# Optimization experiments

Hardware: AMD Instinct MI355X
Metric: run time of the kernel (lower is better)

## Reference

```python
import jax, jax.numpy as jnp
import numpy as np

B, P, D, F = 2048, 16, 1024, 512  # batch, n_prompt, dim, fusion_dim
S = 2 * P  # sequence length
H = D // 2  # classifier hidden
LN_EPS = 1e-5


def _ln_relu(y, g, b):
    mu = jnp.mean(y, axis=-1, keepdims=True)
    var = jnp.mean(jnp.square(y - mu), axis=-1, keepdims=True)
    return jax.nn.relu((y - mu) * jax.lax.rsqrt(var + LN_EPS) * g + b)


def setup_inputs() -> dict:
    key = jax.random.key(0)
    ks = jax.random.split(key, 24)
    n = lambda k, shp, scale: jax.random.normal(k, shp, dtype=jnp.float32) * scale
    return {
        "q": n(ks[0], (B, S, D), 1.0),
        # nn.MultiheadAttention (1 head, batch_first)
        "in_proj_w": n(ks[1], (3 * D, D), 1.0 / np.sqrt(D)),
        "in_proj_b": jnp.zeros((3 * D,), jnp.float32),
        "out_w": n(ks[2], (D, D), 1.0 / np.sqrt(D)),
        "out_b": jnp.zeros((D,), jnp.float32),
        # 32 per-position classifiers, stacked: Linear(D,H)+ReLU+Linear(H,1)+ReLU
        "cls_w1": n(ks[3], (S, H, D), 1.0 / np.sqrt(D)),
        "cls_b1": jnp.zeros((S, H), jnp.float32),
        "cls_w2": n(ks[4], (S, H), 1.0 / np.sqrt(H)),
        "cls_b2": jnp.zeros((S,), jnp.float32),
        # fusion / projector heads: Linear(D,F)+LayerNorm(F)+ReLU
        "fus_w": n(ks[5], (F, D), 1.0 / np.sqrt(D)),
        "fus_b": jnp.zeros((F,), jnp.float32),
        "fus_g": jnp.ones((F,), jnp.float32),
        "fus_be": jnp.zeros((F,), jnp.float32),
        "pa_w": n(ks[6], (F, D), 1.0 / np.sqrt(D)),
        "pa_b": jnp.zeros((F,), jnp.float32),
        "pa_g": jnp.ones((F,), jnp.float32),
        "pa_be": jnp.zeros((F,), jnp.float32),
        "pv_w": n(ks[7], (F, D), 1.0 / np.sqrt(D)),
        "pv_b": jnp.zeros((F,), jnp.float32),
        "pv_g": jnp.ones((F,), jnp.float32),
        "pv_be": jnp.zeros((F,), jnp.float32),
    }


def reference(q, in_proj_w, in_proj_b, out_w, out_b,
              cls_w1, cls_b1, cls_w2, cls_b2,
              fus_w, fus_b, fus_g, fus_be,
              pa_w, pa_b, pa_g, pa_be,
              pv_w, pv_b, pv_g, pv_be):
    # --- single-head self-attention (nn.MultiheadAttention, eval mode) ---
    wq, wk, wv = jnp.split(in_proj_w, 3, axis=0)
    bq, bk, bv = jnp.split(in_proj_b, 3, axis=0)
    qp = jnp.einsum('bsd,ed->bse', q, wq) + bq
    kp = jnp.einsum('bsd,ed->bse', q, wk) + bk
    vp = jnp.einsum('bsd,ed->bse', q, wv) + bv
    scores = jnp.einsum('bse,bte->bst', qp, kp) / jnp.sqrt(jnp.float32(D))
    attn = jax.nn.softmax(scores, axis=-1)
    q_att = jnp.einsum('bst,bte->bse', attn, vp)
    q_att = jnp.einsum('bse,de->bsd', q_att, out_w) + out_b

    # --- per-position tiny classifiers, batched over the 32 slots ---
    h = jax.nn.relu(jnp.einsum('bsd,shd->bsh', q, cls_w1) + cls_b1)  # [B,S,H]
    d = jax.nn.relu(jnp.einsum('bsh,sh->bs', h, cls_w2) + cls_b2)    # [B,S]

    d_a = jax.nn.softmax(d[:, :P], axis=-1)
    d_v = jax.nn.softmax(d[:, P:], axis=-1)
    audio = jnp.einsum('bsd,bs->bd', q_att[:, :P, :], d_a)
    video = jnp.einsum('bsd,bs->bd', q_att[:, P:, :], d_v)
    fusion = (audio + video) * 0.5

    fusion_h = _ln_relu(fusion @ fus_w.T + fus_b, fus_g, fus_be)
    fusion_a = _ln_relu(audio @ pa_w.T + pa_b, pa_g, pa_be)
    fusion_v = _ln_relu(video @ pv_w.T + pv_b, pv_g, pv_be)
    return (fusion_h, fusion_a, fusion_v, d_a, d_v)
```

## Files before the change

kernel.cpp:

```cpp
#include <hip/hip_runtime.h>

#define Bdim 2048
#define Sdim 32
#define Ddim 1024
#define Fdim 512
#define Hdim 512

typedef __bf16 bf16_t;
typedef __bf16 bf16x8 __attribute__((ext_vector_type(8)));
typedef __bf16 bf16x4 __attribute__((ext_vector_type(4)));
typedef float  f32x4  __attribute__((ext_vector_type(4)));

#define BM 128
#define BN 128
#define BK 32

__device__ __forceinline__ void gll16(const bf16_t* g, bf16_t* l) {
  __builtin_amdgcn_global_load_lds((const __attribute__((address_space(1))) void*)g,
                                   (__attribute__((address_space(3))) void*)l,
                                   16, 0, 0);
}

__device__ __forceinline__ int swz32(int row, int k) {
  return row * 32 + (((((k >> 3) ^ ((row >> 1) & 3))) << 3) | (k & 7));
}

__global__ void k_cvt_all(const float* __restrict__ q, const float* __restrict__ ipw,
                          const float* __restrict__ ow, const float* __restrict__ cw1,
                          const float* __restrict__ fusw, const float* __restrict__ paw,
                          const float* __restrict__ pvw,
                          bf16_t* __restrict__ q16, bf16_t* __restrict__ w16,
                          bf16_t* __restrict__ ow16, bf16_t* __restrict__ cls16,
                          bf16_t* __restrict__ hw16) {
  long v = (long)blockIdx.x * 256 + threadIdx.x;
  const float* s; bf16_t* d; long off;
  if (v < 16777216L)      { s = q;    d = q16;            off = 0; }
  else if (v < 17563648L) { s = ipw;  d = w16;            off = 16777216L; }
  else if (v < 17825792L) { s = ow;   d = ow16;           off = 17563648L; }
  else if (v < 22020096L) { s = cw1;  d = cls16;          off = 17825792L; }
  else if (v < 22151168L) { s = fusw; d = hw16;           off = 22020096L; }
  else if (v < 22282240L) { s = paw;  d = hw16 + 524288;  off = 22151168L; }
  else                    { s = pvw;  d = hw16 + 1048576; off = 22282240L; }
  long i = (v - off) * 4;
  float4 t = *(const float4*)(s + i);
  bf16x4 o;
  o[0] = (bf16_t)t.x; o[1] = (bf16_t)t.y; o[2] = (bf16_t)t.z; o[3] = (bf16_t)t.w;
  *(bf16x4*)(d + i) = o;
}

__global__ void k_bias_pre(const float* __restrict__ ipw, const float* __restrict__ ipb,
                           const float* __restrict__ ow, const float* __restrict__ ob,
                           float* __restrict__ u, float* __restrict__ w,
                           float* __restrict__ bp, float* __restrict__ c0) {
  int blk = blockIdx.x, tid = threadIdx.x;
  if (blk < 4) {
    int d = blk * 256 + tid;
    float acc = 0.f;
    #pragma unroll 8
    for (int e = 0; e < Ddim; ++e) acc += ipw[(long)e * Ddim + d] * ipb[Ddim + e];
    u[d] = acc;
  } else if (blk < 8) {
    int d = (blk - 4) * 256 + tid;
    float acc = 0.f;
    #pragma unroll 8
    for (int e = 0; e < Ddim; ++e) acc += ipw[(long)(Ddim + e) * Ddim + d] * ipb[e];
    w[d] = acc;
  } else if (blk < 136) {
    int o = (blk - 8) * 8 + (tid >> 5);
    int l = tid & 31;
    float acc = 0.f;
    #pragma unroll 4
    for (int e = l; e < Ddim; e += 32) acc += ow[(long)o * Ddim + e] * ipb[2 * Ddim + e];
    #pragma unroll
    for (int m = 1; m < 32; m <<= 1) acc += __shfl_xor(acc, m);
    if (l == 0) bp[o] = acc + ob[o];
  } else {
    __shared__ float red[256];
    float acc = 0.f;
    for (int e = tid; e < Ddim; e += 256) acc += ipb[e] * ipb[Ddim + e];
    red[tid] = acc;
    __syncthreads();
    for (int off = 128; off; off >>= 1) {
      if (tid < off) red[tid] += red[tid + off];
      __syncthreads();
    }
    if (tid == 0) c0[0] = red[0];
  }
}

template<int AT, int BT>
__device__ __forceinline__ void gemm_tile(const bf16_t* __restrict__ A, long lda,
                                          const bf16_t* __restrict__ Bt, long ldb,
                                          long m0, long n0, int K,
                                          bf16_t* sa, bf16_t* sb, f32x4 acc[4][4]) {
  const int tid  = threadIdx.x;
  const int wave = tid >> 6;
  const int lane = tid & 63;
  const int quad = lane >> 4;
  const int l16  = lane & 15;
  const int wm = (wave & 1) * 64;
  const int wn = (wave >> 1) * 64;

  for (int kt = 0; kt < K; kt += BK) {
    __syncthreads();
    if constexpr (AT == 0) {
      #pragma unroll
      for (int r = 0; r < 2; ++r) {
        int L = r * 256 + tid;
        int row = L >> 2, cs = L & 3;
        int csrc = cs ^ ((row >> 1) & 3);
        gll16(A + (m0 + row) * lda + kt + csrc * 8, sa + (long)(r * 256 + wave * 64) * 8);
      }
    } else {
      #pragma unroll
      for (int r = 0; r < 2; ++r) {
        int L = r * 256 + tid;
        int gk = L >> 4, gm = (L & 15) * 8;
        bf16x8 v = *(const bf16x8*)(A + (long)(kt + gk) * lda + m0 + gm);
        #pragma unroll
        for (int j = 0; j < 8; ++j) sa[swz32(gm + j, gk)] = v[j];
      }
    }
    if constexpr (BT == 0) {
      #pragma unroll
      for (int r = 0; r < 2; ++r) {
        int L = r * 256 + tid;
        int row = L >> 2, cs = L & 3;
        int csrc = cs ^ ((row >> 1) & 3);
        gll16(Bt + (n0 + row) * ldb + kt + csrc * 8, sb + (long)(r * 256 + wave * 64) * 8);
      }
    } else {
      #pragma unroll
      for (int r = 0; r < 2; ++r) {
        int L = r * 256 + tid;
        int gk = L >> 4, gn = (L & 15) * 8;
        bf16x8 v = *(const bf16x8*)(Bt + (long)(kt + gk) * ldb + n0 + gn);
        #pragma unroll
        for (int j = 0; j < 8; ++j) sb[swz32(gn + j, gk)] = v[j];
      }
    }
    __syncthreads();
    bf16x8 af[4], bfr[4];
    #pragma unroll
    for (int i = 0; i < 4; ++i) {
      int row = wm + i * 16 + l16;
      af[i] = *(const bf16x8*)(sa + row * 32 + ((quad ^ ((row >> 1) & 3)) << 3));
    }
    #pragma unroll
    for (int j = 0; j < 4; ++j) {
      int row = wn + j * 16 + l16;
      bfr[j] = *(const bf16x8*)(sb + row * 32 + ((quad ^ ((row >> 1) & 3)) << 3));
    }
    #pragma unroll
    for (int i = 0; i < 4; ++i)
      #pragma unroll
      for (int j = 0; j < 4; ++j)
        acc[i][j] = __builtin_amdgcn_mfma_f32_16x16x32_bf16(bfr[j], af[i], acc[i][j], 0, 0, 0);
  }
}

template<int AT, int BT>
__global__ __launch_bounds__(256) void k_gemm_bf16(
    const bf16_t* __restrict__ A, long lda, long sAz,
    const bf16_t* __restrict__ Bt, long ldb, long sBz,
    bf16_t* __restrict__ C, long ldc, long sCz,
    const float* __restrict__ bias, int K) {
  __shared__ bf16_t sa[BM * BK];
  __shared__ bf16_t sb[BN * BK];
  long n0 = (long)blockIdx.x * BN;
  long m0 = (long)blockIdx.y * BM;
  long z  = blockIdx.z;
  const bf16_t* Az = A + z * sAz;
  const bf16_t* Bz = Bt + z * sBz;
  bf16_t* Cz = C + z * sCz;
  f32x4 acc[4][4];
  #pragma unroll
  for (int i = 0; i < 4; ++i)
    #pragma unroll
    for (int j = 0; j < 4; ++j) acc[i][j] = (f32x4){0.f, 0.f, 0.f, 0.f};
  gemm_tile<AT, BT>(Az, lda, Bz, ldb, m0, n0, K, sa, sb, acc);
  const int tid = threadIdx.x, wave = tid >> 6, lane = tid & 63;
  const int quad = lane >> 4, l16 = lane & 15;
  const int wm = (wave & 1) * 64, wn = (wave >> 1) * 64;
  #pragma unroll
  for (int i = 0; i < 4; ++i) {
    long row = m0 + wm + i * 16 + l16;
    #pragma unroll
    for (int j = 0; j < 4; ++j) {
      long col = n0 + wn + j * 16 + quad * 4;
      f32x4 b4 = bias ? *(const f32x4*)(bias + col) : (f32x4){0.f, 0.f, 0.f, 0.f};
      bf16x4 o;
      #pragma unroll
      for (int r = 0; r < 4; ++r) o[r] = (bf16_t)(acc[i][j][r] + b4[r]);
      *(bf16x4*)(Cz + row * ldc + col) = o;
    }
  }
}

__global__ __launch_bounds__(256) void k_gemm_f32(
    const bf16_t* __restrict__ A, long lda, long sAz,
    const bf16_t* __restrict__ Bt, long ldb, long sBz,
    float* __restrict__ C, long ldc, long sCz, int K) {
  __shared__ bf16_t sa[BM * BK];
  __shared__ bf16_t sb[BN * BK];
  long n0 = (long)blockIdx.x * BN;
  long m0 = (long)blockIdx.y * BM;
  long z  = blockIdx.z;
  const bf16_t* Az = A + z * sAz;
  const bf16_t* Bz = Bt + z * sBz;
  float* Cz = C + z * sCz;
  f32x4 acc[4][4];
  #pragma unroll
  for (int i = 0; i < 4; ++i)
    #pragma unroll
    for (int j = 0; j < 4; ++j) acc[i][j] = (f32x4){0.f, 0.f, 0.f, 0.f};
  gemm_tile<0, 0>(Az, lda, Bz, ldb, m0, n0, K, sa, sb, acc);
  const int tid = threadIdx.x, wave = tid >> 6, lane = tid & 63;
  const int quad = lane >> 4, l16 = lane & 15;
  const int wm = (wave & 1) * 64, wn = (wave >> 1) * 64;
  #pragma unroll
  for (int i = 0; i < 4; ++i) {
    long row = m0 + wm + i * 16 + l16;
    #pragma unroll
    for (int j = 0; j < 4; ++j) {
      long col = n0 + wn + j * 16 + quad * 4;
      *(f32x4*)(Cz + row * ldc + col) = acc[i][j];
    }
  }
}

__global__ __launch_bounds__(256, 2) void k_gemm_big(
    const bf16_t* __restrict__ A, const bf16_t* __restrict__ Bt,
    bf16_t* __restrict__ C) {
  __shared__ bf16_t sa[128 * 64];
  __shared__ bf16_t sb[256 * 64];
  const int tid = threadIdx.x, wave = tid >> 6, lane = tid & 63;
  const int quad = lane >> 4, l16 = lane & 15;
  int lin = blockIdx.y * 4 + blockIdx.x;
  int c = lin & 7, j0 = lin >> 3;
  long m0 = ((long)c * 64 + (j0 >> 2)) * 128;
  long n0 = (long)(j0 & 3) * 256;
  const int wm = (wave & 1) * 64;
  const int wn = (wave >> 1) * 128;
  f32x4 acc[4][8];
  #pragma unroll
  for (int i = 0; i < 4; ++i)
    #pragma unroll
    for (int j = 0; j < 8; ++j) acc[i][j] = (f32x4){0.f, 0.f, 0.f, 0.f};
  for (int kt = 0; kt < 1024; kt += 64) {
    __syncthreads();
    #pragma unroll
    for (int r = 0; r < 4; ++r) {
      int L = r * 256 + tid;
      int row = L >> 3, cs = L & 7;
      int csrc = cs ^ ((row >> 1) & 7);
      gll16(A + (m0 + row) * 1024 + kt + csrc * 8, sa + (long)(r * 256 + wave * 64) * 8);
    }
    #pragma unroll
    for (int r = 0; r < 8; ++r) {
      int L = r * 256 + tid;
      int row = L >> 3, cs = L & 7;
      int csrc = cs ^ ((row >> 1) & 7);
      gll16(Bt + (n0 + row) * 1024 + kt + csrc * 8, sb + (long)(r * 256 + wave * 64) * 8);
    }
    __syncthreads();
    #pragma unroll
    for (int h = 0; h < 2; ++h) {
      bf16x8 af[4], bfr[8];
      #pragma unroll
      for (int i = 0; i < 4; ++i) {
        int row = wm + i * 16 + l16;
        int cc = h * 4 + quad;
        af[i] = *(const bf16x8*)(sa + row * 64 + ((cc ^ ((row >> 1) & 7)) << 3));
      }
      #pragma unroll
      for (int j = 0; j < 8; ++j) {
        int row = wn + j * 16 + l16;
        int cc = h * 4 + quad;
        bfr[j] = *(const bf16x8*)(sb + row * 64 + ((cc ^ ((row >> 1) & 7)) << 3));
      }
      #pragma unroll
      for (int i = 0; i < 4; ++i)
        #pragma unroll
        for (int j = 0; j < 8; ++j)
          acc[i][j] = __builtin_amdgcn_mfma_f32_16x16x32_bf16(bfr[j], af[i], acc[i][j], 0, 0, 0);
    }
  }
  #pragma unroll
  for (int i = 0; i < 4; ++i) {
    long row = m0 + wm + i * 16 + l16;
    #pragma unroll
    for (int j = 0; j < 8; ++j) {
      long col = n0 + wn + j * 16 + quad * 4;
      bf16x4 o;
      #pragma unroll
      for (int r = 0; r < 4; ++r) o[r] = (bf16_t)(acc[i][j][r]);
      *(bf16x4*)(C + row * 1024 + col) = o;
    }
  }
}

__global__ __launch_bounds__(256) void k_gemm_cls(
    const bf16_t* __restrict__ q16, const bf16_t* __restrict__ w1,
    const float* __restrict__ b1, const float* __restrict__ w2,
    float* __restrict__ dsum) {
  __shared__ bf16_t sa[BM * BK];
  __shared__ bf16_t sb[BN * BK];
  int lin = ((int)blockIdx.z * 16 + blockIdx.y) * 4 + blockIdx.x;
  int c = lin & 7, j0 = lin >> 3;
  int p = c + 8 * (j0 >> 2);
  long n0 = (long)(j0 & 3) * BN;
  int s = p >> 4;
  long m0 = (long)(p & 15) * BM;
  const bf16_t* A  = q16 + (long)s * Ddim;
  const bf16_t* Bt = w1 + (long)s * Hdim * Ddim;
  f32x4 acc[4][4];
  #pragma unroll
  for (int i = 0; i < 4; ++i)
    #pragma unroll
    for (int j = 0; j < 4; ++j) acc[i][j] = (f32x4){0.f, 0.f, 0.f, 0.f};
  gemm_tile<0, 0>(A, (long)Sdim * Ddim, Bt, Ddim, m0, n0, Ddim, sa, sb, acc);
  const int tid = threadIdx.x, wave = tid >> 6, lane = tid & 63;
  const int quad = lane >> 4, l16 = lane & 15;
  const int wm = (wave & 1) * 64, wn = (wave >> 1) * 64;
  const float* b1s = b1 + (long)s * Hdim;
  const float* w2s = w2 + (long)s * Hdim;
  #pragma unroll
  for (int i = 0; i < 4; ++i) {
    float vsum = 0.f;
    #pragma unroll
    for (int j = 0; j < 4; ++j) {
      long col = n0 + wn + j * 16 + quad * 4;
      f32x4 b4 = *(const f32x4*)(b1s + col);
      f32x4 w4 = *(const f32x4*)(w2s + col);
      #pragma unroll
      for (int r = 0; r < 4; ++r)
        vsum += fmaxf(acc[i][j][r] + b4[r], 0.f) * w4[r];
    }
    vsum += __shfl_xor(vsum, 16);
    vsum += __shfl_xor(vsum, 32);
    if (lane < 16) {
      long row = m0 + wm + i * 16 + l16;
      atomicAdd(&dsum[row * Sdim + s], vsum);
    }
  }
}

__global__ void k_finalize_d(const float* __restrict__ dsum, const float* __restrict__ cb2,
                             float* __restrict__ daws, float* __restrict__ out_da,
                             float* __restrict__ out_dv) {
  int t = blockIdx.x * 256 + threadIdx.x;
  int b = t >> 5, s = t & 31;
  float v = fmaxf(dsum[t] + cb2[s], 0.f);
  float m = v;
  #pragma unroll
  for (int mask = 1; mask < 16; mask <<= 1) m = fmaxf(m, __shfl_xor(m, mask));
  float e = __expf(v - m);
  float sum = e;
  #pragma unroll
  for (int mask = 1; mask < 16; mask <<= 1) sum += __shfl_xor(sum, mask);
  float r = e / sum;
  daws[t] = r;
  if (s < 16) out_da[b * 16 + s] = r;
  else        out_dv[b * 16 + (s - 16)] = r;
}

#define QPAD 264
__global__ __launch_bounds__(256) void k_attn_pool(
    const bf16_t* __restrict__ q16, const bf16_t* __restrict__ G16,
    const float* __restrict__ daws, const float* __restrict__ u,
    const float* __restrict__ wv, const float* __restrict__ c0p,
    bf16_t* __restrict__ pooled) {
  __shared__ bf16_t qc[32 * QPAD];
  __shared__ bf16_t gc[32 * QPAD];
  __shared__ float sc[32][33];
  __shared__ float qup[32][8], qwp[32][8];
  __shared__ float quL[32], qwL[32], caL[32], cvL[32], daL[16], dvL[16];
  const int tid = threadIdx.x, wave = tid >> 6, lane = tid & 63;
  const int quad = lane >> 4, l16 = lane & 15;
  const long b = blockIdx.x;
  const bf16_t* qb = q16 + b * (Sdim * Ddim);
  const bf16_t* gb = G16 + b * (Sdim * Ddim);
  if (tid < 32) {
    float dval = daws[b * Sdim + tid];
    if (tid < 16) daL[tid] = dval; else dvL[tid - 16] = dval;
  }
  qup[tid >> 3][tid & 7] = 0.f;
  qwp[tid >> 3][tid & 7] = 0.f;
  const int ti = wave & 1, tj = wave >> 1;
  f32x4 acc = (f32x4){0.f, 0.f, 0.f, 0.f};
  for (int kc = 0; kc < Ddim; kc += 256) {
    __syncthreads();
    #pragma unroll
    for (int r = 0; r < 4; ++r) {
      int L = r * 256 + tid;
      int row = L >> 5, koff = (L & 31) * 8;
      *(bf16x8*)(qc + row * QPAD + koff) = *(const bf16x8*)(qb + (long)row * Ddim + kc + koff);
      *(bf16x8*)(gc + row * QPAD + koff) = *(const bf16x8*)(gb + (long)row * Ddim + kc + koff);
    }
    __syncthreads();
    #pragma unroll
    for (int kk = 0; kk < 8; ++kk) {
      bf16x8 a  = *(const bf16x8*)(gc + (ti * 16 + l16) * QPAD + kk * 32 + quad * 8);
      bf16x8 bb = *(const bf16x8*)(qc + (tj * 16 + l16) * QPAD + kk * 32 + quad * 8);
      acc = __builtin_amdgcn_mfma_f32_16x16x32_bf16(a, bb, acc, 0, 0, 0);
    }
    {
      int s2 = tid & 31, sl = tid >> 5;
      float pu = 0.f, pw = 0.f;
      const bf16_t* qrow = qc + s2 * QPAD + sl * 32;
      const float* ub = u + kc + sl * 32;
      const float* wb = wv + kc + sl * 32;
      #pragma unroll
      for (int kb = 0; kb < 4; ++kb) {
        bf16x8 qv = *(const bf16x8*)(qrow + kb * 8);
        f32x4 u0 = *(const f32x4*)(ub + kb * 8);
        f32x4 u1 = *(const f32x4*)(ub + kb * 8 + 4);
        f32x4 w0 = *(const f32x4*)(wb + kb * 8);
        f32x4 w1 = *(const f32x4*)(wb + kb * 8 + 4);
        #pragma unroll
        for (int e = 0; e < 4; ++e) {
          pu += (float)qv[e] * u0[e] + (float)qv[e + 4] * u1[e];
          pw += (float)qv[e] * w0[e] + (float)qv[e + 4] * w1[e];
        }
      }
      qup[s2][sl] += pu;
      qwp[s2][sl] += pw;
    }
  }
  __syncthreads();
  if (tid < 32) {
    float a0 = 0.f, a1 = 0.f;
    for (int k = 0; k < 8; ++k) { a0 += qup[tid][k]; a1 += qwp[tid][k]; }
    quL[tid] = a0; qwL[tid] = a1;
  }
  __syncthreads();
  {
    float c00 = c0p[0];
    int col = tj * 16 + l16;
    #pragma unroll
    for (int r = 0; r < 4; ++r) {
      int row = ti * 16 + quad * 4 + r;
      sc[row][col] = (acc[r] + quL[row] + qwL[col] + c00) * 0.03125f;
    }
  }
  __syncthreads();
  if (tid < 32) {
    float mx = -1e30f;
    for (int t = 0; t < 32; ++t) mx = fmaxf(mx, sc[tid][t]);
    float sum = 0.f;
    for (int t = 0; t < 32; ++t) { float e = __expf(sc[tid][t] - mx); sc[tid][t] = e; sum += e; }
    float inv = 1.f / sum;
    for (int t = 0; t < 32; ++t) sc[tid][t] *= inv;
  }
  __syncthreads();
  if (tid < 32) {
    float a0 = 0.f, a1 = 0.f;
    for (int s2 = 0; s2 < 16; ++s2) a0 += daL[s2] * sc[s2][tid];
    for (int s2 = 0; s2 < 16; ++s2) a1 += dvL[s2] * sc[16 + s2][tid];
    caL[tid] = a0; cvL[tid] = a1;
  }
  __syncthreads();
  {
    int d0 = tid * 4;
    float ap[4] = {0.f, 0.f, 0.f, 0.f}, vp[4] = {0.f, 0.f, 0.f, 0.f};
    for (int t = 0; t < 32; ++t) {
      float ca = caL[t], cv = cvL[t];
      bf16x4 qv = *(const bf16x4*)(qb + (long)t * Ddim + d0);
      #pragma unroll
      for (int e = 0; e < 4; ++e) {
        float x = (float)qv[e];
        ap[e] += ca * x;
        vp[e] += cv * x;
      }
    }
    bf16x4 pf, pa, pv;
    #pragma unroll
    for (int e = 0; e < 4; ++e) {
      pf[e] = (bf16_t)(0.5f * (ap[e] + vp[e]));
      pa[e] = (bf16_t)ap[e];
      pv[e] = (bf16_t)vp[e];
    }
    *(bf16x4*)(pooled + b * 3072 + d0)        = pf;
    *(bf16x4*)(pooled + b * 3072 + 1024 + d0) = pa;
    *(bf16x4*)(pooled + b * 3072 + 2048 + d0) = pv;
  }
}

__global__ __launch_bounds__(256) void k_ln(
    const float* __restrict__ Y,
    const float* __restrict__ fb, const float* __restrict__ fg, const float* __restrict__ fbe,
    const float* __restrict__ ab, const float* __restrict__ ag, const float* __restrict__ abe,
    const float* __restrict__ vb, const float* __restrict__ vg, const float* __restrict__ vbe,
    float* __restrict__ out) {
  int wave = threadIdx.x >> 6, lane = threadIdx.x & 63;
  long row = (long)blockIdx.x * 4 + wave;
  int head = (int)(row >> 11);
  const float* bb = (head == 0) ? fb : (head == 1) ? ab : vb;
  const float* gg = (head == 0) ? fg : (head == 1) ? ag : vg;
  const float* be = (head == 0) ? fbe : (head == 1) ? abe : vbe;
  const float* y = Y + row * Fdim + lane * 8;
  float v[8];
  float s = 0.f;
  #pragma unroll
  for (int k = 0; k < 8; ++k) { v[k] = y[k] + bb[lane * 8 + k]; s += v[k]; }
  #pragma unroll
  for (int m = 1; m < 64; m <<= 1) s += __shfl_xor(s, m);
  float mu = s * (1.f / Fdim);
  float vs = 0.f;
  #pragma unroll
  for (int k = 0; k < 8; ++k) { float t = v[k] - mu; vs += t * t; }
  #pragma unroll
  for (int m = 1; m < 64; m <<= 1) vs += __shfl_xor(vs, m);
  float inv = rsqrtf(vs * (1.f / Fdim) + 1e-5f);
  float* o = out + row * Fdim + lane * 8;
  #pragma unroll
  for (int k = 0; k < 8; ++k) {
    float t = (v[k] - mu) * inv * gg[lane * 8 + k] + be[lane * 8 + k];
    o[k] = fmaxf(t, 0.f);
  }
}

extern "C" void kernel_launch(void* const* d_in, const int* in_sizes, int n_in,
                              void* d_out, int out_size, void* d_ws, size_t ws_size,
                              hipStream_t stream) {
  const float* q    = (const float*)d_in[0];
  const float* ipw  = (const float*)d_in[1];
  const float* ipb  = (const float*)d_in[2];
  const float* ow   = (const float*)d_in[3];
  const float* ob   = (const float*)d_in[4];
  const float* cw1  = (const float*)d_in[5];
  const float* cb1  = (const float*)d_in[6];
  const float* cw2  = (const float*)d_in[7];
  const float* cb2  = (const float*)d_in[8];
  const float* fusw = (const float*)d_in[9];
  const float* fusb = (const float*)d_in[10];
  const float* fusg = (const float*)d_in[11];
  const float* fusbe= (const float*)d_in[12];
  const float* paw  = (const float*)d_in[13];
  const float* pab  = (const float*)d_in[14];
  const float* pag  = (const float*)d_in[15];
  const float* pabe = (const float*)d_in[16];
  const float* pvw  = (const float*)d_in[17];
  const float* pvb  = (const float*)d_in[18];
  const float* pvg  = (const float*)d_in[19];
  const float* pvbe = (const float*)d_in[20];
  float* out = (float*)d_out;

  const size_t o_q16   = 0;
  const size_t o_w16   = 134217728;
  const size_t o_ow16  = 140509184;
  const size_t o_cls16 = 142606336;
  const size_t o_hw16  = 176160768;
  const size_t o_Mt    = 179306496;
  const size_t o_Nt    = 181403648;
  const size_t o_G16   = 183500800;
  const size_t o_pool  = 317718528;
  const size_t o_u     = 330301440;
  const size_t o_wv    = 330305536;
  const size_t o_bp    = 330309632;
  const size_t o_c0    = 330313728;
  const size_t o_dsum  = 330313984;
  const size_t o_daws  = 330576128;
  const size_t total   = 330838272;
  if (ws_size < total) return;

  char* ws = (char*)d_ws;
  bf16_t* q16   = (bf16_t*)(ws + o_q16);
  bf16_t* w16   = (bf16_t*)(ws + o_w16);
  bf16_t* Wq16  = w16;
  bf16_t* Wk16  = w16 + 1048576;
  bf16_t* Wv16  = w16 + 2097152;
  bf16_t* ow16  = (bf16_t*)(ws + o_ow16);
  bf16_t* cls16 = (bf16_t*)(ws + o_cls16);
  bf16_t* hw16  = (bf16_t*)(ws + o_hw16);
  bf16_t* Mt    = (bf16_t*)(ws + o_Mt);
  bf16_t* Nt    = (bf16_t*)(ws + o_Nt);
  bf16_t* G16   = (bf16_t*)(ws + o_G16);
  bf16_t* S116  = (bf16_t*)(ws + o_G16);
  float*  Yf    = (float*)(ws + o_G16 + 12582912);
  bf16_t* pool16= (bf16_t*)(ws + o_pool);
  float*  uf    = (float*)(ws + o_u);
  float*  wvf   = (float*)(ws + o_wv);
  float*  bpf   = (float*)(ws + o_bp);
  float*  c0f   = (float*)(ws + o_c0);
  float*  dsum  = (float*)(ws + o_dsum);
  float*  daws  = (float*)(ws + o_daws);

  k_cvt_all<<<dim3(87552), dim3(256), 0, stream>>>(
      q, ipw, ow, cw1, fusw, paw, pvw, q16, w16, ow16, cls16, hw16);

  k_bias_pre<<<dim3(137), dim3(256), 0, stream>>>(ipw, ipb, ow, ob, uf, wvf, bpf, c0f);

  k_gemm_bf16<1, 1><<<dim3(8, 8, 1), dim3(256), 0, stream>>>(
      Wk16, Ddim, 0, Wq16, Ddim, 0, Mt, Ddim, 0, nullptr, Ddim);

  k_gemm_bf16<0, 1><<<dim3(8, 8, 1), dim3(256), 0, stream>>>(
      ow16, Ddim, 0, Wv16, Ddim, 0, Nt, Ddim, 0, nullptr, Ddim);

  k_gemm_big<<<dim3(4, 512), dim3(256), 0, stream>>>(q16, Mt, G16);

  hipMemsetAsync(dsum, 0, (size_t)Bdim * Sdim * sizeof(float), stream);
  k_gemm_cls<<<dim3(4, 16, 32), dim3(256), 0, stream>>>(q16, cls16, cb1, cw2, dsum);

  k_finalize_d<<<dim3(256), dim3(256), 0, stream>>>(
      dsum, cb2, daws, out + 3145728, out + 3145728 + 32768);

  k_attn_pool<<<dim3(2048), dim3(256), 0, stream>>>(q16, G16, daws, uf, wvf, c0f, pool16);

  k_gemm_bf16<0, 0><<<dim3(8, 48, 1), dim3(256), 0, stream>>>(
      pool16, Ddim, 0, Nt, Ddim, 0, S116, Ddim, 0, bpf, Ddim);

  k_gemm_f32<<<dim3(4, 16, 3), dim3(256), 0, stream>>>(
      S116, 3L * Ddim, Ddim, hw16, Ddim, (long)Fdim * Ddim,
      Yf, Fdim, (long)Bdim * Fdim, Ddim);

  k_ln<<<dim3(1536), dim3(256), 0, stream>>>(
      Yf, fusb, fusg, fusbe, pab, pag, pabe, pvb, pvg, pvbe, out);
}
```

Baseline: 1.030 ms.

## Restructure big GEMM into 256x256 tiles with triple-buffered async LDS pipeline

Rewrites k_gemm_big to use 512-thread blocks computing 256x256 output tiles with BK=32 and three LDS buffers. Global-to-LDS loads for future k-steps are issued ahead, with partial vmcnt waits, so memory latency overlaps MFMA compute. The main loop also uses one barrier per stage instead of two and raises wave priority around the MFMA block. The larger tile raises arithmetic intensity, at the cost of more accumulator registers per thread and fewer blocks in the grid.

After: 1.043 ms. About the same (+1.3%).

```diff
diff --git a/kernel.cpp b/kernel.cpp
--- a/kernel.cpp
+++ b/kernel.cpp
@@ -229,68 +229,101 @@
   }
 }
 
-__global__ __launch_bounds__(256, 2) void k_gemm_big(
+__global__ __launch_bounds__(512, 2) void k_gemm_big(
     const bf16_t* __restrict__ A, const bf16_t* __restrict__ Bt,
     bf16_t* __restrict__ C) {
-  __shared__ bf16_t sa[128 * 64];
-  __shared__ bf16_t sb[256 * 64];
+  __shared__ bf16_t sa[3][256 * 32];
+  __shared__ bf16_t sb[3][256 * 32];
   const int tid = threadIdx.x, wave = tid >> 6, lane = tid & 63;
   const int quad = lane >> 4, l16 = lane & 15;
-  int lin = blockIdx.y * 4 + blockIdx.x;
-  int c = lin & 7, j0 = lin >> 3;
-  long m0 = ((long)c * 64 + (j0 >> 2)) * 128;
-  long n0 = (long)(j0 & 3) * 256;
-  const int wm = (wave & 1) * 64;
-  const int wn = (wave >> 1) * 128;
-  f32x4 acc[4][8];
-  #pragma unroll
-  for (int i = 0; i < 4; ++i)
-    #pragma unroll
-    for (int j = 0; j < 8; ++j) acc[i][j] = (f32x4){0.f, 0.f, 0.f, 0.f};
-  for (int kt = 0; kt < 1024; kt += 64) {
-    __syncthreads();
-    #pragma unroll
-    for (int r = 0; r < 4; ++r) {
-      int L = r * 256 + tid;
-      int row = L >> 3, cs = L & 7;
-      int csrc = cs ^ ((row >> 1) & 7);
-      gll16(A + (m0 + row) * 1024 + kt + csrc * 8, sa + (long)(r * 256 + wave * 64) * 8);
-    }
-    #pragma unroll
-    for (int r = 0; r < 8; ++r) {
-      int L = r * 256 + tid;
-      int row = L >> 3, cs = L & 7;
-      int csrc = cs ^ ((row >> 1) & 7);
-      gll16(Bt + (n0 + row) * 1024 + kt + csrc * 8, sb + (long)(r * 256 + wave * 64) * 8);
-    }
-    __syncthreads();
-    #pragma unroll
-    for (int h = 0; h < 2; ++h) {
-      bf16x8 af[4], bfr[8];
-      #pragma unroll
-      for (int i = 0; i < 4; ++i) {
-        int row = wm + i * 16 + l16;
-        int cc = h * 4 + quad;
-        af[i] = *(const bf16x8*)(sa + row * 64 + ((cc ^ ((row >> 1) & 7)) << 3));
-      }
-      #pragma unroll
-      for (int j = 0; j < 8; ++j) {
-        int row = wn + j * 16 + l16;
-        int cc = h * 4 + quad;
-        bfr[j] = *(const bf16x8*)(sb + row * 64 + ((cc ^ ((row >> 1) & 7)) << 3));
-      }
-      #pragma unroll
-      for (int i = 0; i < 4; ++i)
-        #pragma unroll
-        for (int j = 0; j < 8; ++j)
-          acc[i][j] = __builtin_amdgcn_mfma_f32_16x16x32_bf16(bfr[j], af[i], acc[i][j], 0, 0, 0);
-    }
-  }
-  #pragma unroll
-  for (int i = 0; i < 4; ++i) {
+  int lin = blockIdx.x;
+  int c = lin & 7, t0 = lin >> 3;
+  int wg = c * 128 + t0;
+  long m0 = (long)(wg >> 2) * 256;
+  long n0 = (long)(wg & 3) * 256;
+  const int wm = (wave >> 2) * 128;
+  const int wn = (wave & 3) * 64;
+  const int rowS = tid >> 2, cs = tid & 3;
+  const int csrcS = cs ^ ((rowS >> 1) & 3);
+  const bf16_t* Abase = A + (m0 + rowS) * 1024 + csrcS * 8;
+  const bf16_t* Bbase = Bt + (n0 + rowS) * 1024 + csrcS * 8;
+  const int dst0 = wave * 512;
+  const int dst1 = 4096 + wave * 512;
+
+  f32x4 acc[8][4];
+  #pragma unroll
+  for (int i = 0; i < 8; ++i)
+    #pragma unroll
+    for (int j = 0; j < 4; ++j) acc[i][j] = (f32x4){0.f, 0.f, 0.f, 0.f};
+
+#define GB_STAGE(KT, BUF)                                    \
+  do {                                                       \
+    const bf16_t* Ab = Abase + (KT);                         \
+    const bf16_t* Bb = Bbase + (KT);                         \
+    gll16(Ab,              sa[BUF] + dst0);                  \
+    gll16(Ab + 128 * 1024, sa[BUF] + dst1);                  \
+    gll16(Bb,              sb[BUF] + dst0);                  \
+    gll16(Bb + 128 * 1024, sb[BUF] + dst1);                  \
+  } while (0)
+
+#define GB_COMPUTE(BUF)                                                            \
+  do {                                                                             \
+    bf16x8 af[8], bfr[4];                                                          \
+    _Pragma("unroll")                                                              \
+    for (int i = 0; i < 8; ++i) {                                                  \
+      int row = wm + i * 16 + l16;                                                 \
+      af[i] = *(const bf16x8*)(&sa[BUF][row * 32 + ((quad ^ ((row >> 1) & 3)) << 3)]); \
+    }                                                                              \
+    _Pragma("unroll")                                                              \
+    for (int j = 0; j < 4; ++j) {                                                  \
+      int row = wn + j * 16 + l16;                                                 \
+      bfr[j] = *(const bf16x8*)(&sb[BUF][row * 32 + ((quad ^ ((row >> 1) & 3)) << 3)]); \
+    }                                                                              \
+    __builtin_amdgcn_s_setprio(1);                                                 \
+    _Pragma("unroll")                                                              \
+    for (int i = 0; i < 8; ++i)                                                    \
+      _Pragma("unroll")                                                            \
+      for (int j = 0; j < 4; ++j)                                                  \
+        acc[i][j] = __builtin_amdgcn_mfma_f32_16x16x32_bf16(bfr[j], af[i], acc[i][j], 0, 0, 0); \
+    __builtin_amdgcn_s_setprio(0);                                                 \
+  } while (0)
+
+#define GB_SYNC(N)                                           \
+  asm volatile("s_waitcnt vmcnt(" #N ")" ::: "memory");      \
+  __builtin_amdgcn_s_barrier();                              \
+  asm volatile("" ::: "memory")
+
+  GB_STAGE(0, 0);
+  GB_STAGE(32, 1);
+
+  int kt = 64;
+  #pragma unroll 1
+  for (int g = 0; g < 10; ++g) {
+    GB_SYNC(4);
+    GB_STAGE(kt, 2);
+    GB_COMPUTE(0);
+    GB_SYNC(4);
+    GB_STAGE(kt + 32, 0);
+    GB_COMPUTE(1);
+    GB_SYNC(4);
+    GB_STAGE(kt + 64, 1);
+    GB_COMPUTE(2);
+    kt += 96;
+  }
+  GB_SYNC(4);
+  GB_COMPUTE(0);
+  GB_SYNC(0);
+  GB_COMPUTE(1);
+
+#undef GB_STAGE
+#undef GB_COMPUTE
+#undef GB_SYNC
+
+  #pragma unroll
+  for (int i = 0; i < 8; ++i) {
     long row = m0 + wm + i * 16 + l16;
     #pragma unroll
-    for (int j = 0; j < 8; ++j) {
+    for (int j = 0; j < 4; ++j) {
       long col = n0 + wn + j * 16 + quad * 4;
       bf16x4 o;
       #pragma unroll
@@ -598,7 +631,7 @@
   k_gemm_bf16<0, 1><<<dim3(8, 8, 1), dim3(256), 0, stream>>>(
       ow16, Ddim, 0, Wv16, Ddim, 0, Nt, Ddim, 0, nullptr, Ddim);
 
-  k_gemm_big<<<dim3(4, 512), dim3(256), 0, stream>>>(q16, Mt, G16);
+  k_gemm_big<<<dim3(1024), dim3(512), 0, stream>>>(q16, Mt, G16);
 
   hipMemsetAsync(dsum, 0, (size_t)Bdim * Sdim * sizeof(float), stream);
   k_gemm_cls<<<dim3(4, 16, 32), dim3(256), 0, stream>>>(q16, cls16, cb1, cw2, dsum);
```
